# Performance work log

Measured on AMD Instinct MI355X. Metric: run time of the kernel, lower is better.

The kernel has to match this reference:

```python
import jax, jax.numpy as jnp
import numpy as np

EMA_A = 0.4      # exponential moving average decay used in Hash_ExpMovAverage
WIN = 9          # window_size
LN_EPS = 1e-3    # keras LayerNormalization default epsilon


def setup_inputs() -> dict:
    key = jax.random.key(0)
    ks = jax.random.split(key, 8)
    B, N, D, H = 8, 4096, 256, 8
    w = lambda k, shape: jax.random.normal(k, shape, jnp.float32) * 0.05
    return {
        "x": jax.random.normal(ks[0], (B, N, D), jnp.float32),
        "head_kernel": w(ks[1], (D, H, D)),
        "head_bias": w(ks[2], (H, D)),
        "down_kernel": w(ks[3], (H, D, D)),
        "down_bias": w(ks[4], (D,)),
        "value_kernel": w(ks[5], (D, D)),
        "value_bias": w(ks[6], (D,)),
        "ln_gamma": jnp.ones((D,), jnp.float32),
        "ln_beta": jnp.zeros((D,), jnp.float32),
    }


def reference(x, head_kernel, head_bias, down_kernel, down_bias,
              value_kernel, value_bias, ln_gamma, ln_beta):
    B, N, D = x.shape
    half = (WIN - 1) // 2

    # Up_Projection: [B,N,D] -> [B,N,H,D], relu
    q = jax.nn.relu(jnp.einsum('bnd,dhe->bnhe', x, head_kernel) + head_bias)

    # ---- Neighborhoods_Arrangement ----
    # Neighborhood_SimHash: sign codes from relu activations, summed over heads
    codes = 2.0 * jnp.minimum(jnp.ceil(q), 1.0) - 1.0        # [B,N,H,D]
    lsh = jnp.sum(codes, axis=-2)                            # [B,N,D]
    # Hash_ExpMovAverage: sort descending along D, add positional encoding, EMA dot
    pos = jnp.argsort(-lsh, axis=-1)                         # descending order
    lsh_sorted = jnp.take_along_axis(lsh, pos, axis=-1)
    pf = pos.astype(jnp.float32)
    freq = 10.0 ** (-(pf / jnp.float32(D)))                  # 1 / 10**powers
    pe = jnp.sin(freq) * (pf % 2) + jnp.cos(freq) * (1.0 - pf % 2)
    vals = lsh_sorted + pe / EMA_A
    c = EMA_A * (1.0 - EMA_A) ** jnp.arange(D, dtype=jnp.float32)
    simv = jnp.einsum('bnd,d->bn', vals, c)                  # [B,N]
    order = jnp.argsort(simv, axis=-1)                       # ascending
    q = jnp.take_along_axis(q, order[:, :, None, None], axis=1)  # reorder tokens

    # Down_Projection: [B,N,H,D] -> [B,N,D], relu
    q = jax.nn.relu(jnp.einsum('bnhd,hde->bne', q, down_kernel) + down_bias)

    # (matches tile-first / extract_patches / tile-last concat in the original)
    starts = jnp.clip(jnp.arange(N) - half, 0, N - WIN)      # [N]
    widx = starts[:, None] + jnp.arange(WIN)[None, :]
    keyw = q[:, widx]

    scale = jnp.sqrt(jnp.float32(D))
    scores = jax.nn.softmax(jnp.einsum('bnd,bnwd->bnw', q, keyw) / scale, axis=-1)
    value = jax.nn.relu(jnp.einsum('bnwd,de->bnwe', keyw, value_kernel) + value_bias)
    attn_out = jnp.einsum('bnwd,bnw->bnd', value, scores)

    # Residual with ORIGINAL (un-permuted) inputs + LayerNorm (keras default eps)
    y = attn_out + x
    mu = jnp.mean(y, axis=-1, keepdims=True)
    var = jnp.var(y, axis=-1, keepdims=True)
    return (y - mu) / jnp.sqrt(var + LN_EPS) * ln_gamma + ln_beta
```

## Files before the change

### kernel.cpp

```cpp
#include <hip/hip_runtime.h>

constexpr int Bc = 8, Nc = 4096, Dc = 256, Hc = 8;
constexpr int TN = 16;
constexpr int XS = 20;
constexpr int TN3 = 32;
constexpr int XS3 = 36;

using short8 = __attribute__((ext_vector_type(8))) short;
using f32x4  = __attribute__((ext_vector_type(4))) float;

static __device__ __forceinline__ unsigned short f2bf(float f) {
    unsigned u = __float_as_uint(f);
    u += 0x7fffu + ((u >> 16) & 1u);
    return (unsigned short)(u >> 16);
}

__global__ __launch_bounds__(256)
void k0_wdt(const float* __restrict__ Wd, unsigned short* __restrict__ WdT)
{
    __shared__ float tile[64][65];
    const int h  = blockIdx.x >> 4;
    const int t  = blockIdx.x & 15;
    const int kb = (t >> 2) * 64, eb = (t & 3) * 64;
    const int tid = threadIdx.x;
    {
        const int krow = tid >> 2, ec = (tid & 3) * 16;
        const float* src = Wd + h * 65536 + (kb + krow) * 256 + eb + ec;
        #pragma unroll
        for (int i = 0; i < 4; ++i) {
            float4 v = *reinterpret_cast<const float4*>(src + i * 4);
            tile[krow][ec + i * 4 + 0] = v.x;
            tile[krow][ec + i * 4 + 1] = v.y;
            tile[krow][ec + i * 4 + 2] = v.z;
            tile[krow][ec + i * 4 + 3] = v.w;
        }
    }
    __syncthreads();
    {
        const int erow = tid >> 2, dc = (tid & 3) * 16;
        unsigned short o[16];
        #pragma unroll
        for (int i = 0; i < 16; ++i) o[i] = f2bf(tile[dc + i][erow]);
        unsigned short* dst = WdT + h * 65536 + (eb + erow) * 256 + kb + dc;
        *reinterpret_cast<short8*>(dst)     = *reinterpret_cast<short8*>(&o[0]);
        *reinterpret_cast<short8*>(dst + 8) = *reinterpret_cast<short8*>(&o[8]);
    }
}

__global__ __launch_bounds__(256, 4)
void k1_head_down(const float* __restrict__ x,
                  const float* __restrict__ Wh, const float* __restrict__ bh,
                  const unsigned short* __restrict__ WdT, const float* __restrict__ bd,
                  float* __restrict__ z, float* __restrict__ simv)
{
    __shared__ float xT[256 * XS];
    __shared__ unsigned short qTb[TN * 256];
    __shared__ signed char lshL[256 * 17];
    __shared__ float pe_over[256];
    __shared__ float c_f[256];
    __shared__ int   cnt_l[TN * 16];

    const int tid = threadIdx.x;
    const long rowbase = (long)blockIdx.x * TN;

    {
        const int d = tid;
        const float u = -((float)d * 0.00390625f);
        const float freq = (float)pow(10.0, (double)u);
        const float pe = (d & 1) ? (float)sin((double)freq)
                                 : (float)cos((double)freq);
        pe_over[d] = __fdiv_rn(pe, 0.4f);
        c_f[d] = __fmul_rn(0.4f, (float)pow((double)0.6f, (double)d));
    }
    #pragma unroll
    for (int r = 0; r < TN; ++r)
        xT[tid * XS + r] = x[(rowbase + r) * 256 + tid];

    int lshv[TN];
    #pragma unroll
    for (int r = 0; r < TN; ++r) lshv[r] = 0;

    const int wavei = tid >> 6, lane = tid & 63;
    const int mrow = lane & 15, kgrp = lane >> 4;
    f32x4 acc[4];
    #pragma unroll
    for (int nf = 0; nf < 4; ++nf) acc[nf] = (f32x4){0.f, 0.f, 0.f, 0.f};

    __syncthreads();

    for (int h = 0; h < Hc; ++h) {
        float accq[TN];
        #pragma unroll
        for (int r = 0; r < TN; ++r) accq[r] = 0.0f;
        const float* wcol = Wh + h * 256 + tid;
        float wb[8];
        #pragma unroll
        for (int i = 0; i < 8; ++i) wb[i] = wcol[i * 2048];
        for (int k0 = 0; k0 < 256; k0 += 8) {
            float wn[8];
            const bool more = (k0 + 8) < 256;
            if (more) {
                #pragma unroll
                for (int i = 0; i < 8; ++i) wn[i] = wcol[(k0 + 8 + i) * 2048];
            }
            #pragma unroll
            for (int i = 0; i < 8; ++i) {
                const float* xk = &xT[(k0 + i) * XS];
                const float w = wb[i];
                #pragma unroll
                for (int r4 = 0; r4 < TN; r4 += 4) {
                    float4 xv = *reinterpret_cast<const float4*>(xk + r4);
                    accq[r4 + 0] = fmaf(xv.x, w, accq[r4 + 0]);
                    accq[r4 + 1] = fmaf(xv.y, w, accq[r4 + 1]);
                    accq[r4 + 2] = fmaf(xv.z, w, accq[r4 + 2]);
                    accq[r4 + 3] = fmaf(xv.w, w, accq[r4 + 3]);
                }
            }
            if (more) {
                #pragma unroll
                for (int i = 0; i < 8; ++i) wb[i] = wn[i];
            }
        }
        const float bias = bh[h * 256 + tid];
        __syncthreads();
        #pragma unroll
        for (int r = 0; r < TN; ++r) {
            const float pre = __fadd_rn(accq[r], bias);
            lshv[r] += (pre > 0.0f) ? 1 : -1;
            qTb[r * 256 + tid] = f2bf(fmaxf(pre, 0.0f));
        }
        __syncthreads();
        const unsigned short* wdh = WdT + h * 65536;
        #pragma unroll 2
        for (int ks = 0; ks < 8; ++ks) {
            short8 af = *reinterpret_cast<const short8*>(&qTb[mrow * 256 + ks * 32 + kgrp * 8]);
            #pragma unroll
            for (int nf = 0; nf < 4; ++nf) {
                const int e = wavei * 64 + nf * 16 + mrow;
                short8 bf = *reinterpret_cast<const short8*>(&wdh[e * 256 + ks * 32 + kgrp * 8]);
                acc[nf] = __builtin_amdgcn_mfma_f32_16x16x32_bf16(af, bf, acc[nf], 0, 0, 0);
            }
        }
    }
    #pragma unroll
    for (int nf = 0; nf < 4; ++nf) {
        const int e = wavei * 64 + nf * 16 + mrow;
        const float b = bd[e];
        #pragma unroll
        for (int reg = 0; reg < 4; ++reg) {
            const int m = kgrp * 4 + reg;
            z[(rowbase + m) * 256 + e] = fmaxf(acc[nf][reg] + b, 0.0f);
        }
    }
    #pragma unroll
    for (int r = 0; r < TN; ++r)
        lshL[tid * 17 + r] = (signed char)lshv[r];
    __syncthreads();
    if (tid < TN) {
        const int r = tid;
        int* cw = &cnt_l[r * 16];
        for (int i = 0; i < 9; ++i) cw[i] = 0;
        for (int d = 0; d < 256; ++d) {
            int vv = (int)lshL[d * 17 + r];
            cw[(vv + 8) >> 1] += 1;
        }
        int run = 0;
        for (int bin = 8; bin >= 0; --bin) { int c0 = cw[bin]; cw[bin] = run; run += c0; }
        float* valq = &xT[r * 256];
        for (int d = 0; d < 256; ++d) {
            int vv = (int)lshL[d * 17 + r];
            int bin = (vv + 8) >> 1;
            int j = cw[bin]++;
            valq[j] = __fadd_rn((float)vv, pe_over[d]);
        }
        float L0 = 0.f, L1 = 0.f, L2 = 0.f, L3 = 0.f,
              L4 = 0.f, L5 = 0.f, L6 = 0.f, L7 = 0.f;
        for (int i = 0; i < 256; i += 8) {
            L0 = fmaf(valq[i + 0], c_f[i + 0], L0);
            L1 = fmaf(valq[i + 1], c_f[i + 1], L1);
            L2 = fmaf(valq[i + 2], c_f[i + 2], L2);
            L3 = fmaf(valq[i + 3], c_f[i + 3], L3);
            L4 = fmaf(valq[i + 4], c_f[i + 4], L4);
            L5 = fmaf(valq[i + 5], c_f[i + 5], L5);
            L6 = fmaf(valq[i + 6], c_f[i + 6], L6);
            L7 = fmaf(valq[i + 7], c_f[i + 7], L7);
        }
        const float h0 = __fadd_rn(L0, L4);
        const float h1 = __fadd_rn(L1, L5);
        const float h2 = __fadd_rn(L2, L6);
        const float h3 = __fadd_rn(L3, L7);
        simv[rowbase + r] = __fadd_rn(__fadd_rn(h0, h2), __fadd_rn(h1, h3));
    }
}

__global__ __launch_bounds__(256)
void k2_rank(const float* __restrict__ simv, int* __restrict__ order)
{
    __shared__ float s_l[4096];
    const int b = blockIdx.x >> 4;
    const int chunk = blockIdx.x & 15;
    const float* S = simv + (long)b * 4096;
    for (int i = threadIdx.x; i < 4096; i += 256) s_l[i] = S[i];
    __syncthreads();
    const int n = chunk * 256 + threadIdx.x;
    const float key = s_l[n];
    int cnt = 0;
    for (int m = 0; m < 4096; ++m) {
        float sm = s_l[m];
        cnt += (sm < key) ? 1 : ((sm == key && m < n) ? 1 : 0);
    }
    order[(long)b * 4096 + cnt] = n;
}

__global__ __launch_bounds__(256, 2)
void k3_value(const float* __restrict__ z, const int* __restrict__ order,
              const float* __restrict__ Wv, const float* __restrict__ bv,
              float* __restrict__ v)
{
    __shared__ float zT[256 * XS3];
    __shared__ int sh_ord[TN3];
    const int tid = threadIdx.x;
    const long rowbase = (long)blockIdx.x * TN3;
    const long bbase = (rowbase >> 12) << 12;
    if (tid < TN3) sh_ord[tid] = order[rowbase + tid];
    __syncthreads();
    #pragma unroll
    for (int r = 0; r < TN3; ++r)
        zT[tid * XS3 + r] = z[(bbase + sh_ord[r]) * 256 + tid];
    float acc[TN3];
    #pragma unroll
    for (int r = 0; r < TN3; ++r) acc[r] = 0.0f;
    __syncthreads();
    const float* wc = Wv + tid;
    #pragma unroll 2
    for (int k = 0; k < 256; ++k) {
        float w = wc[k * 256];
        const float* zk = &zT[k * XS3];
        #pragma unroll
        for (int r4 = 0; r4 < TN3; r4 += 4) {
            float4 zv = *reinterpret_cast<const float4*>(zk + r4);
            acc[r4 + 0] = fmaf(zv.x, w, acc[r4 + 0]);
            acc[r4 + 1] = fmaf(zv.y, w, acc[r4 + 1]);
            acc[r4 + 2] = fmaf(zv.z, w, acc[r4 + 2]);
            acc[r4 + 3] = fmaf(zv.w, w, acc[r4 + 3]);
        }
    }
    const float bias = bv[tid];
    #pragma unroll
    for (int r = 0; r < TN3; ++r)
        v[(rowbase + r) * 256 + tid] = fmaxf(acc[r] + bias, 0.0f);
}

__global__ __launch_bounds__(256)
void k4_attn_ln(const float* __restrict__ z, const float* __restrict__ v,
                const int* __restrict__ order, const float* __restrict__ x,
                const float* __restrict__ gamma, const float* __restrict__ beta,
                float* __restrict__ out)
{
    const int tid = threadIdx.x;
    const int wv = tid >> 6, lane = tid & 63;
    const long row = (long)blockIdx.x * 4 + wv;
    const int n = (int)(row & 4095);
    const long bbase = row - n;
    int start = n - 4;
    start = start < 0 ? 0 : start;
    start = start > (Nc - 9) ? (Nc - 9) : start;
    const int d0 = lane * 4;

    const int srcq = order[bbase + n];
    float4 q4 = *reinterpret_cast<const float4*>(&z[(bbase + srcq) * 256 + d0]);

    float t[9];
    #pragma unroll
    for (int w = 0; w < 9; ++w) {
        int srcm = order[bbase + start + w];
        float4 kv = *reinterpret_cast<const float4*>(&z[(bbase + srcm) * 256 + d0]);
        float p = q4.x * kv.x + q4.y * kv.y + q4.z * kv.z + q4.w * kv.w;
        #pragma unroll
        for (int off = 32; off > 0; off >>= 1) p += __shfl_xor(p, off);
        t[w] = p * 0.0625f;
    }
    float mx = t[0];
    #pragma unroll
    for (int w = 1; w < 9; ++w) mx = fmaxf(mx, t[w]);
    float pw[9], psum = 0.0f;
    #pragma unroll
    for (int w = 0; w < 9; ++w) { pw[w] = expf(t[w] - mx); psum += pw[w]; }
    const float pinv = 1.0f / psum;

    float4 a = make_float4(0.f, 0.f, 0.f, 0.f);
    #pragma unroll
    for (int w = 0; w < 9; ++w) {
        float4 vv = *reinterpret_cast<const float4*>(&v[(bbase + start + w) * 256 + d0]);
        float s = pw[w] * pinv;
        a.x = fmaf(vv.x, s, a.x);
        a.y = fmaf(vv.y, s, a.y);
        a.z = fmaf(vv.z, s, a.z);
        a.w = fmaf(vv.w, s, a.w);
    }
    float4 xv = *reinterpret_cast<const float4*>(&x[(bbase + n) * 256 + d0]);
    float4 y = make_float4(a.x + xv.x, a.y + xv.y, a.z + xv.z, a.w + xv.w);

    float s1 = y.x + y.y + y.z + y.w;
    float s2 = y.x * y.x + y.y * y.y + y.z * y.z + y.w * y.w;
    #pragma unroll
    for (int off = 32; off > 0; off >>= 1) {
        s1 += __shfl_xor(s1, off);
        s2 += __shfl_xor(s2, off);
    }
    const float mu = s1 * (1.0f / 256.0f);
    const float var = s2 * (1.0f / 256.0f) - mu * mu;
    const float istd = 1.0f / sqrtf(var + 0.001f);

    float4 g4 = *reinterpret_cast<const float4*>(&gamma[d0]);
    float4 b4 = *reinterpret_cast<const float4*>(&beta[d0]);
    float4 o;
    o.x = (y.x - mu) * istd * g4.x + b4.x;
    o.y = (y.y - mu) * istd * g4.y + b4.y;
    o.z = (y.z - mu) * istd * g4.z + b4.z;
    o.w = (y.w - mu) * istd * g4.w + b4.w;
    *reinterpret_cast<float4*>(&out[row * 256 + d0]) = o;
}

extern "C" void kernel_launch(void* const* d_in, const int* in_sizes, int n_in,
                              void* d_out, int out_size, void* d_ws, size_t ws_size,
                              hipStream_t stream)
{
    const float* x  = (const float*)d_in[0];
    const float* Wh = (const float*)d_in[1];
    const float* bh = (const float*)d_in[2];
    const float* Wd = (const float*)d_in[3];
    const float* bd = (const float*)d_in[4];
    const float* Wv = (const float*)d_in[5];
    const float* bv = (const float*)d_in[6];
    const float* g  = (const float*)d_in[7];
    const float* be = (const float*)d_in[8];
    float* out = (float*)d_out;

    char* ws = (char*)d_ws;
    float*          z     = (float*)ws;
    float*          v     = (float*)(ws + 33554432);
    float*          simv  = (float*)(ws + 67108864);
    int*            order = (int*)(ws + 67239936);
    unsigned short* WdT   = (unsigned short*)(ws + 67371008);

    const int rows = Bc * Nc;
    k0_wdt<<<dim3(128), dim3(256), 0, stream>>>(Wd, WdT);
    k1_head_down<<<dim3(rows / TN), dim3(256), 0, stream>>>(x, Wh, bh, WdT, bd, z, simv);
    k2_rank<<<dim3(Bc * 16), dim3(256), 0, stream>>>(simv, order);
    k3_value<<<dim3(rows / TN3), dim3(256), 0, stream>>>(z, order, Wv, bv, v);
    k4_attn_ln<<<dim3(rows / 4), dim3(256), 0, stream>>>(z, v, order, x, g, be, out);
}
```

Before: 926.2 us.

## Compute head projection with split-bf16 MFMA and exact fp32 fixup near zero

The fp32 scalar-FMA head projection is replaced by MFMA bf16 matrix ops. x and Wh are each split into high and low bf16 parts and multiplied with four MFMAs to approximate fp32 accuracy. Outputs whose pre-activation is close to zero are logged and recomputed in exact fp32 afterwards, so the sign-based hash codes stay correct. This removes the dominant scalar FMA cost, at the price of a weight-split preprocessing kernel, extra LDS use that lowers the occupancy hint, and a fallback list that may overflow its 1024 slots.

Result: slower. 1.147 ms (+23.8%).

```diff
diff --git a/kernel.cpp b/kernel.cpp
--- a/kernel.cpp
+++ b/kernel.cpp
@@ -2,7 +2,6 @@
 
 constexpr int Bc = 8, Nc = 4096, Dc = 256, Hc = 8;
 constexpr int TN = 16;
-constexpr int XS = 20;
 constexpr int TN3 = 32;
 constexpr int XS3 = 36;
 
@@ -13,6 +12,12 @@
     unsigned u = __float_as_uint(f);
     u += 0x7fffu + ((u >> 16) & 1u);
     return (unsigned short)(u >> 16);
+}
+static __device__ __forceinline__ float bf2f(unsigned short h) {
+    return __uint_as_float(((unsigned)h) << 16);
+}
+static __device__ __forceinline__ int swz(int r, int k) {
+    return (r << 9) + ((k << 1) ^ ((r & 7) << 4));
 }
 
 __global__ __launch_bounds__(256)
@@ -47,21 +52,69 @@
     }
 }
 
-__global__ __launch_bounds__(256, 4)
+__global__ __launch_bounds__(256)
+void k0_whsplit(const float* __restrict__ Wh,
+                unsigned short* __restrict__ WhH, unsigned short* __restrict__ WhL)
+{
+    __shared__ float tile[64][65];
+    const int h  = blockIdx.x >> 4;
+    const int t  = blockIdx.x & 15;
+    const int kb = (t >> 2) * 64, eb = (t & 3) * 64;
+    const int tid = threadIdx.x;
+    {
+        const int krow = tid >> 2, ec = (tid & 3) * 16;
+        const float* src = Wh + (kb + krow) * 2048 + h * 256 + eb + ec;
+        #pragma unroll
+        for (int i = 0; i < 4; ++i) {
+            float4 v = *reinterpret_cast<const float4*>(src + i * 4);
+            tile[krow][ec + i * 4 + 0] = v.x;
+            tile[krow][ec + i * 4 + 1] = v.y;
+            tile[krow][ec + i * 4 + 2] = v.z;
+            tile[krow][ec + i * 4 + 3] = v.w;
+        }
+    }
+    __syncthreads();
+    {
+        const int erow = tid >> 2, dc = (tid & 3) * 16;
+        unsigned short oh[16], ol[16];
+        #pragma unroll
+        for (int i = 0; i < 16; ++i) {
+            float v = tile[dc + i][erow];
+            unsigned short hi = f2bf(v);
+            oh[i] = hi;
+            ol[i] = f2bf(v - bf2f(hi));
+        }
+        const long base = (long)h * 65536 + (eb + erow) * 256 + kb + dc;
+        *reinterpret_cast<short8*>(WhH + base)     = *reinterpret_cast<short8*>(&oh[0]);
+        *reinterpret_cast<short8*>(WhH + base + 8) = *reinterpret_cast<short8*>(&oh[8]);
+        *reinterpret_cast<short8*>(WhL + base)     = *reinterpret_cast<short8*>(&ol[0]);
+        *reinterpret_cast<short8*>(WhL + base + 8) = *reinterpret_cast<short8*>(&ol[8]);
+    }
+}
+
+#define XSH_OFF 0
+#define XSL_OFF 8192
+#define QTB_OFF 16384
+#define LSH_OFF 24576
+#define PE_OFF  40960
+#define CF_OFF  41984
+#define CNT_OFF 43008
+#define FCN_OFF 44032
+#define FLS_OFF 44048
+
+__global__ __launch_bounds__(256, 3)
 void k1_head_down(const float* __restrict__ x,
                   const float* __restrict__ Wh, const float* __restrict__ bh,
+                  const unsigned short* __restrict__ WhH, const unsigned short* __restrict__ WhL,
                   const unsigned short* __restrict__ WdT, const float* __restrict__ bd,
                   float* __restrict__ z, float* __restrict__ simv)
 {
-    __shared__ float xT[256 * XS];
-    __shared__ unsigned short qTb[TN * 256];
-    __shared__ signed char lshL[256 * 17];
-    __shared__ float pe_over[256];
-    __shared__ float c_f[256];
-    __shared__ int   cnt_l[TN * 16];
+    __shared__ __align__(16) char SM[49152];
 
     const int tid = threadIdx.x;
     const long rowbase = (long)blockIdx.x * TN;
+    const int wavei = tid >> 6, lane = tid & 63;
+    const int mrow = lane & 15, kgrp = lane >> 4;
 
     {
         const int d = tid;
@@ -69,78 +122,96 @@
         const float freq = (float)pow(10.0, (double)u);
         const float pe = (d & 1) ? (float)sin((double)freq)
                                  : (float)cos((double)freq);
-        pe_over[d] = __fdiv_rn(pe, 0.4f);
-        c_f[d] = __fmul_rn(0.4f, (float)pow((double)0.6f, (double)d));
-    }
-    #pragma unroll
-    for (int r = 0; r < TN; ++r)
-        xT[tid * XS + r] = x[(rowbase + r) * 256 + tid];
-
-    int lshv[TN];
-    #pragma unroll
-    for (int r = 0; r < TN; ++r) lshv[r] = 0;
-
-    const int wavei = tid >> 6, lane = tid & 63;
-    const int mrow = lane & 15, kgrp = lane >> 4;
-    f32x4 acc[4];
-    #pragma unroll
-    for (int nf = 0; nf < 4; ++nf) acc[nf] = (f32x4){0.f, 0.f, 0.f, 0.f};
+        ((float*)(SM + PE_OFF))[d] = __fdiv_rn(pe, 0.4f);
+        ((float*)(SM + CF_OFF))[d] = __fmul_rn(0.4f, (float)pow((double)0.6f, (double)d));
+    }
+    if (tid == 0) *((int*)(SM + FCN_OFF)) = 0;
+    {
+        const int r = tid >> 4, kc = (tid & 15) * 16;
+        const float* src = x + (rowbase + r) * 256 + kc;
+        unsigned short oh[16], ol[16];
+        #pragma unroll
+        for (int i = 0; i < 16; i += 4) {
+            float4 v = *reinterpret_cast<const float4*>(src + i);
+            float vv[4] = {v.x, v.y, v.z, v.w};
+            #pragma unroll
+            for (int j = 0; j < 4; ++j) {
+                unsigned short hi = f2bf(vv[j]);
+                oh[i + j] = hi;
+                ol[i + j] = f2bf(vv[j] - bf2f(hi));
+            }
+        }
+        *reinterpret_cast<short8*>(SM + XSH_OFF + swz(r, kc))     = *reinterpret_cast<short8*>(&oh[0]);
+        *reinterpret_cast<short8*>(SM + XSH_OFF + swz(r, kc + 8)) = *reinterpret_cast<short8*>(&oh[8]);
+        *reinterpret_cast<short8*>(SM + XSL_OFF + swz(r, kc))     = *reinterpret_cast<short8*>(&ol[0]);
+        *reinterpret_cast<short8*>(SM + XSL_OFF + swz(r, kc + 8)) = *reinterpret_cast<short8*>(&ol[8]);
+    }
+
+    int lshv[16];
+    #pragma unroll
+    for (int i = 0; i < 16; ++i) lshv[i] = 0;
+    f32x4 dacc[4];
+    #pragma unroll
+    for (int nf = 0; nf < 4; ++nf) dacc[nf] = (f32x4){0.f, 0.f, 0.f, 0.f};
 
     __syncthreads();
 
     for (int h = 0; h < Hc; ++h) {
-        float accq[TN];
-        #pragma unroll
-        for (int r = 0; r < TN; ++r) accq[r] = 0.0f;
-        const float* wcol = Wh + h * 256 + tid;
-        float wb[8];
-        #pragma unroll
-        for (int i = 0; i < 8; ++i) wb[i] = wcol[i * 2048];
-        for (int k0 = 0; k0 < 256; k0 += 8) {
-            float wn[8];
-            const bool more = (k0 + 8) < 256;
-            if (more) {
-                #pragma unroll
-                for (int i = 0; i < 8; ++i) wn[i] = wcol[(k0 + 8 + i) * 2048];
-            }
-            #pragma unroll
-            for (int i = 0; i < 8; ++i) {
-                const float* xk = &xT[(k0 + i) * XS];
-                const float w = wb[i];
-                #pragma unroll
-                for (int r4 = 0; r4 < TN; r4 += 4) {
-                    float4 xv = *reinterpret_cast<const float4*>(xk + r4);
-                    accq[r4 + 0] = fmaf(xv.x, w, accq[r4 + 0]);
-                    accq[r4 + 1] = fmaf(xv.y, w, accq[r4 + 1]);
-                    accq[r4 + 2] = fmaf(xv.z, w, accq[r4 + 2]);
-                    accq[r4 + 3] = fmaf(xv.w, w, accq[r4 + 3]);
-                }
-            }
-            if (more) {
-                #pragma unroll
-                for (int i = 0; i < 8; ++i) wb[i] = wn[i];
-            }
-        }
-        const float bias = bh[h * 256 + tid];
-        __syncthreads();
-        #pragma unroll
-        for (int r = 0; r < TN; ++r) {
-            const float pre = __fadd_rn(accq[r], bias);
-            lshv[r] += (pre > 0.0f) ? 1 : -1;
-            qTb[r * 256 + tid] = f2bf(fmaxf(pre, 0.0f));
-        }
-        __syncthreads();
-        const unsigned short* wdh = WdT + h * 65536;
+        f32x4 hacc[4];
+        #pragma unroll
+        for (int nf = 0; nf < 4; ++nf) hacc[nf] = (f32x4){0.f, 0.f, 0.f, 0.f};
+        const unsigned short* whh = WhH + (long)h * 65536;
+        const unsigned short* whl = WhL + (long)h * 65536;
         #pragma unroll 2
-        for (int ks = 0; ks < 8; ++ks) {
-            short8 af = *reinterpret_cast<const short8*>(&qTb[mrow * 256 + ks * 32 + kgrp * 8]);
+        for (int kt = 0; kt < 8; ++kt) {
+            const int k0 = kt * 32 + kgrp * 8;
+            short8 afh = *reinterpret_cast<const short8*>(SM + XSH_OFF + swz(mrow, k0));
+            short8 afl = *reinterpret_cast<const short8*>(SM + XSL_OFF + swz(mrow, k0));
             #pragma unroll
             for (int nf = 0; nf < 4; ++nf) {
                 const int e = wavei * 64 + nf * 16 + mrow;
-                short8 bf = *reinterpret_cast<const short8*>(&wdh[e * 256 + ks * 32 + kgrp * 8]);
-                acc[nf] = __builtin_amdgcn_mfma_f32_16x16x32_bf16(af, bf, acc[nf], 0, 0, 0);
+                short8 bfh = *reinterpret_cast<const short8*>(&whh[e * 256 + k0]);
+                short8 bfl = *reinterpret_cast<const short8*>(&whl[e * 256 + k0]);
+                hacc[nf] = __builtin_amdgcn_mfma_f32_16x16x32_bf16(afh, bfh, hacc[nf], 0, 0, 0);
+                hacc[nf] = __builtin_amdgcn_mfma_f32_16x16x32_bf16(afh, bfl, hacc[nf], 0, 0, 0);
+                hacc[nf] = __builtin_amdgcn_mfma_f32_16x16x32_bf16(afl, bfh, hacc[nf], 0, 0, 0);
+                hacc[nf] = __builtin_amdgcn_mfma_f32_16x16x32_bf16(afl, bfl, hacc[nf], 0, 0, 0);
             }
         }
+        #pragma unroll
+        for (int nf = 0; nf < 4; ++nf) {
+            const int e = wavei * 64 + nf * 16 + mrow;
+            const float bias = bh[h * 256 + e];
+            #pragma unroll
+            for (int reg = 0; reg < 4; ++reg) {
+                const int r = kgrp * 4 + reg;
+                const float pre = __fadd_rn(hacc[nf][reg], bias);
+                const int s = (pre > 0.0f) ? 1 : -1;
+                lshv[nf * 4 + reg] += s;
+                if (fabsf(pre) < 2e-3f) {
+                    int idx = atomicAdd((int*)(SM + FCN_OFF), 1);
+                    if (idx < 1024)
+                        ((int*)(SM + FLS_OFF))[idx] =
+                            r | (e << 4) | (h << 12) | ((s > 0 ? 1 : 0) << 15);
+                }
+                *reinterpret_cast<unsigned short*>(SM + QTB_OFF + swz(r, e)) =
+                    f2bf(fmaxf(pre, 0.0f));
+            }
+        }
+        __syncthreads();
+        const unsigned short* wdh = WdT + (long)h * 65536;
+        #pragma unroll 2
+        for (int ks = 0; ks < 8; ++ks) {
+            const int k0 = ks * 32 + kgrp * 8;
+            short8 af = *reinterpret_cast<const short8*>(SM + QTB_OFF + swz(mrow, k0));
+            #pragma unroll
+            for (int nf = 0; nf < 4; ++nf) {
+                const int e = wavei * 64 + nf * 16 + mrow;
+                short8 bf = *reinterpret_cast<const short8*>(&wdh[e * 256 + k0]);
+                dacc[nf] = __builtin_amdgcn_mfma_f32_16x16x32_bf16(af, bf, dacc[nf], 0, 0, 0);
+            }
+        }
+        __syncthreads();
     }
     #pragma unroll
     for (int nf = 0; nf < 4; ++nf) {
@@ -149,26 +220,55 @@
         #pragma unroll
         for (int reg = 0; reg < 4; ++reg) {
             const int m = kgrp * 4 + reg;
-            z[(rowbase + m) * 256 + e] = fmaxf(acc[nf][reg] + b, 0.0f);
-        }
-    }
-    #pragma unroll
-    for (int r = 0; r < TN; ++r)
-        lshL[tid * 17 + r] = (signed char)lshv[r];
+            z[(rowbase + m) * 256 + e] = fmaxf(dacc[nf][reg] + b, 0.0f);
+        }
+    }
+    {
+        int* lshI = (int*)(SM + LSH_OFF);
+        #pragma unroll
+        for (int nf = 0; nf < 4; ++nf) {
+            const int e = wavei * 64 + nf * 16 + mrow;
+            #pragma unroll
+            for (int reg = 0; reg < 4; ++reg)
+                lshI[e * 16 + kgrp * 4 + reg] = lshv[nf * 4 + reg];
+        }
+    }
+    __syncthreads();
+    {
+        int n = *((int*)(SM + FCN_OFF));
+        n = n < 1024 ? n : 1024;
+        for (int i = tid; i < n; i += 256) {
+            const int ent = ((int*)(SM + FLS_OFF))[i];
+            const int r = ent & 15, e = (ent >> 4) & 255, h = (ent >> 12) & 7;
+            const int fs = ((ent >> 15) & 1) ? 1 : -1;
+            const float* xr = x + (rowbase + r) * 256;
+            const float* wcol = Wh + h * 256 + e;
+            float acc = 0.0f;
+            for (int k = 0; k < 256; ++k)
+                acc = fmaf(xr[k], wcol[k * 2048], acc);
+            const float pre = __fadd_rn(acc, bh[h * 256 + e]);
+            const int es = (pre > 0.0f) ? 1 : -1;
+            if (es != fs)
+                atomicAdd(&((int*)(SM + LSH_OFF))[e * 16 + r], es - fs);
+        }
+    }
     __syncthreads();
     if (tid < TN) {
         const int r = tid;
-        int* cw = &cnt_l[r * 16];
+        const int* lshI = (const int*)(SM + LSH_OFF);
+        const float* pe_over = (const float*)(SM + PE_OFF);
+        const float* c_f = (const float*)(SM + CF_OFF);
+        int* cw = (int*)(SM + CNT_OFF) + r * 16;
         for (int i = 0; i < 9; ++i) cw[i] = 0;
         for (int d = 0; d < 256; ++d) {
-            int vv = (int)lshL[d * 17 + r];
+            int vv = lshI[d * 16 + r];
             cw[(vv + 8) >> 1] += 1;
         }
         int run = 0;
         for (int bin = 8; bin >= 0; --bin) { int c0 = cw[bin]; cw[bin] = run; run += c0; }
-        float* valq = &xT[r * 256];
+        float* valq = (float*)(SM + r * 1024);
         for (int d = 0; d < 256; ++d) {
-            int vv = (int)lshL[d * 17 + r];
+            int vv = lshI[d * 16 + r];
             int bin = (vv + 8) >> 1;
             int j = cw[bin]++;
             valq[j] = __fadd_rn((float)vv, pe_over[d]);
@@ -343,10 +443,13 @@
     float*          simv  = (float*)(ws + 67108864);
     int*            order = (int*)(ws + 67239936);
     unsigned short* WdT   = (unsigned short*)(ws + 67371008);
+    unsigned short* WhH   = (unsigned short*)(ws + 68419584);
+    unsigned short* WhL   = (unsigned short*)(ws + 69468160);
 
     const int rows = Bc * Nc;
     k0_wdt<<<dim3(128), dim3(256), 0, stream>>>(Wd, WdT);
-    k1_head_down<<<dim3(rows / TN), dim3(256), 0, stream>>>(x, Wh, bh, WdT, bd, z, simv);
+    k0_whsplit<<<dim3(128), dim3(256), 0, stream>>>(Wh, WhH, WhL);
+    k1_head_down<<<dim3(rows / TN), dim3(256), 0, stream>>>(x, Wh, bh, WhH, WhL, WdT, bd, z, simv);
     k2_rank<<<dim3(Bc * 16), dim3(256), 0, stream>>>(simv, order);
     k3_value<<<dim3(rows / TN3), dim3(256), 0, stream>>>(z, order, Wv, bv, v);
     k4_attn_ln<<<dim3(rows / 4), dim3(256), 0, stream>>>(z, v, order, x, g, be, out);
```
